# Kernel optimization log

Hardware: AMD Instinct MI355X
Metric: run time of the kernel (lower is better)

Reference implementation:

```python
import jax, jax.numpy as jnp
import numpy as np

H = 2048      # hidden_size
DM = 4096     # intermediate_size
N = 16        # ssm state size
K = 4         # conv kernel
R = 128       # time_step_rank
B_SZ = 1
L = 1024


def setup_inputs() -> dict:
    key = jax.random.key(0)
    ks = jax.random.split(key, 10)
    s = 0.02
    hidden_states = jax.random.normal(ks[0], (B_SZ, L, H), dtype=jnp.float32)
    W_in = jax.random.normal(ks[1], (2 * DM, H), dtype=jnp.float32) * s
    conv_w = jax.random.normal(ks[2], (DM, 1, K), dtype=jnp.float32) * 0.3
    conv_b = jax.random.normal(ks[3], (DM,), dtype=jnp.float32) * 0.1
    W_x = jax.random.normal(ks[4], (R + 2 * N, DM), dtype=jnp.float32) * s
    W_dt = jax.random.normal(ks[5], (DM, R), dtype=jnp.float32) * s
    b_dt = jax.random.normal(ks[6], (DM,), dtype=jnp.float32) * 0.1
    # A_log init: log(arange(1..N)) broadcast over channels (per __init__)
    A_log = jnp.broadcast_to(jnp.log(jnp.arange(1, N + 1, dtype=jnp.float32))[None, :], (DM, N)).copy()
    D_param = jnp.ones((DM,), dtype=jnp.float32)
    W_out = jax.random.normal(ks[7], (H, DM), dtype=jnp.float32) * s
    return {"hidden_states": hidden_states, "W_in": W_in, "conv_w": conv_w,
            "conv_b": conv_b, "W_x": W_x, "W_dt": W_dt, "b_dt": b_dt,
            "A_log": A_log, "D_param": D_param, "W_out": W_out}


def reference(hidden_states, W_in, conv_w, conv_b, W_x, W_dt, b_dt, A_log, D_param, W_out):
    # in_proj then chunk into hidden / gate (torch chunks dim=1 after transpose)
    proj = hidden_states @ W_in.T                     # [B, L, 2D]
    h, gate = proj[..., :DM], proj[..., DM:]          # each [B, L, D]
    # depthwise causal conv1d, padding K-1 then truncate to L (left-pad == same)
    h_cl = jnp.transpose(h, (0, 2, 1))                # [B, D, L]
    hc = jax.lax.conv_general_dilated(
        h_cl, conv_w, window_strides=(1,), padding=[(K - 1, 0)],
        dimension_numbers=("NCH", "OIH", "NCH"), feature_group_count=DM)
    hc = jax.nn.silu(hc + conv_b[None, :, None])      # [B, D, L]
    hc_ld = jnp.transpose(hc, (0, 2, 1))              # [B, L, D]
    # x_proj -> dt, B, C
    ssm_p = hc_ld @ W_x.T                             # [B, L, R+2N]
    ts, Bm, Cm = ssm_p[..., :R], ssm_p[..., R:R + N], ssm_p[..., R + N:]
    dt = jax.nn.softplus(ts @ W_dt.T + b_dt)          # [B, L, D]
    A = -jnp.exp(A_log)                               # [D, N]
    dA = jnp.exp(dt[:, :, :, None] * A[None, None, :, :])            # [B, L, D, N]
    dBu = dt[:, :, :, None] * Bm[:, :, None, :] * hc_ld[:, :, :, None]  # [B, L, D, N]
    # selective scan over time: state = dA*state + dBu; y = <state, C>
    def step(state, inp):
        dA_t, dBu_t, C_t = inp                        # [B,D,N],[B,D,N],[B,N]
        state = dA_t * state + dBu_t
        y = jnp.einsum("bdn,bn->bd", state, C_t)
        return state, y
    init = jnp.zeros((hidden_states.shape[0], DM, N), dtype=hidden_states.dtype)
    _, ys = jax.lax.scan(step, init,
                         (jnp.swapaxes(dA, 0, 1), jnp.swapaxes(dBu, 0, 1), jnp.swapaxes(Cm, 0, 1)))
    y = jnp.transpose(ys, (1, 0, 2))                  # [B, L, D]
    y = y + hc_ld * D_param[None, None, :]            # skip via D
    y = y * jax.nn.silu(gate)                         # gating
    return y @ W_out.T                                # [B, L, H]
```

## Files before the change

kernel.cpp:

```cpp
#include <hip/hip_runtime.h>
#include <math.h>

#define AS1 __attribute__((address_space(1)))
#define AS3 __attribute__((address_space(3)))

typedef __attribute__((ext_vector_type(8))) short short8;
typedef __attribute__((ext_vector_type(4))) float f32x4;

#define WAITV(n) asm volatile("s_waitcnt vmcnt(" #n ")" ::: "memory")
#define LGKM0()  asm volatile("s_waitcnt lgkmcnt(0)" ::: "memory")
#define BARRIER() asm volatile("s_barrier" ::: "memory")
#define SCHEDB() __builtin_amdgcn_sched_barrier(0)

static __device__ __forceinline__ unsigned short f2bf(float f) {
    unsigned u = __float_as_uint(f);
    unsigned r = (u + 0x7fffu + ((u >> 16) & 1u)) >> 16;
    return (unsigned short)r;
}
static __device__ __forceinline__ float bf2f(unsigned short u) {
    return __uint_as_float(((unsigned)u) << 16);
}

__global__ __launch_bounds__(256) void cvt_f32_bf16(const float* __restrict__ src,
                                                    unsigned short* __restrict__ dst,
                                                    int n4) {
    int i = blockIdx.x * 256 + threadIdx.x;
    int stride = gridDim.x * 256;
    for (; i < n4; i += stride) {
        float4 v = ((const float4*)src)[i];
        ushort4 o;
        o.x = f2bf(v.x); o.y = f2bf(v.y); o.z = f2bf(v.z); o.w = f2bf(v.w);
        ((ushort4*)dst)[i] = o;
    }
}

__global__ __launch_bounds__(256) void cvt_ts(const float* __restrict__ ssmp,
                                              unsigned short* __restrict__ ts) {
    int i = blockIdx.x * 256 + threadIdx.x;
    int t = i >> 5, c4 = (i & 31) * 4;
    float4 v = *(const float4*)&ssmp[t * 160 + c4];
    ushort4 o;
    o.x = f2bf(v.x); o.y = f2bf(v.y); o.z = f2bf(v.z); o.w = f2bf(v.w);
    *(ushort4*)&ts[t * 128 + c4] = o;
}

__global__ __launch_bounds__(256) void conv_silu(const float* __restrict__ h,
                                                 const float* __restrict__ cw,
                                                 const float* __restrict__ cb,
                                                 unsigned short* __restrict__ hc_bf) {
    int idx = blockIdx.x * 256 + threadIdx.x;
    int d = idx & 4095, t = idx >> 12;
    float acc = cb[d];
    float4 w = *(const float4*)&cw[d * 4];
    const float* wp = (const float*)&w;
#pragma unroll
    for (int k = 0; k < 4; ++k) {
        int tt = t + k - 3;
        if (tt >= 0) acc += h[tt * 4096 + d] * wp[k];
    }
    float s = acc / (1.f + __expf(-acc));
    hc_bf[idx] = f2bf(s);
}

__global__ __launch_bounds__(256) void reduce4(const float* __restrict__ pA,
                                               const float* __restrict__ pB,
                                               float* __restrict__ out, int n4) {
    int i = blockIdx.x * 256 + threadIdx.x;
    int stride = gridDim.x * 256;
    const size_t MN4 = (size_t)1024 * 2048 / 4;
    for (; i < n4; i += stride) {
        float4 a = ((const float4*)pA)[i];
        float4 b = ((const float4*)pA)[i + MN4];
        float4 c = ((const float4*)pB)[i];
        float4 d = ((const float4*)pB)[i + MN4];
        float4 o;
        o.x = (a.x + b.x) + (c.x + d.x);
        o.y = (a.y + b.y) + (c.y + d.y);
        o.z = (a.z + b.z) + (c.z + d.z);
        o.w = (a.w + b.w) + (c.w + d.w);
        ((float4*)out)[i] = o;
    }
}

enum { P_GATE = 0, P_PART = 1 };

template <int EPI>
__global__ __launch_bounds__(512, 2)
void gemm8p(const short* __restrict__ A, const short* __restrict__ B,
            void* __restrict__ C0v, void* __restrict__ C1v,
            int N, int K, int kchunk) {
    __shared__ short lds[3 * 24576];

    const int tid = threadIdx.x;
    const int wv = tid >> 6, ln = tid & 63;
    const int lr = ln & 15, kg = ln >> 4;
    const int wm = wv >> 2, wn = wv & 3;

    const int nwg = gridDim.x;
    const int bid = blockIdx.x;
    const int swz = (bid & 7) * (nwg >> 3) + (bid >> 3);
    const int by = swz & 7, bx = swz >> 3;
    const int m0 = by * 128;
    const int n0 = bx * 256;
    const int kbeg = blockIdx.z * kchunk;
    const int NT = kchunk >> 6;

    f32x4 acc[4][4];
#pragma unroll
    for (int mi = 0; mi < 4; ++mi)
#pragma unroll
        for (int ni = 0; ni < 4; ++ni) acc[mi][ni] = (f32x4){0.f, 0.f, 0.f, 0.f};

    const short* Abase = A + (size_t)m0 * K + kbeg;
    const short* Bbase = B + (size_t)n0 * K + kbeg;

#define STAGE_A(kt, b)                                                        \
    {                                                                         \
        short* lbase = &lds[(b) * 24576];                                     \
        _Pragma("unroll")                                                     \
        for (int r = 0; r < 2; ++r) {                                         \
            int c = r * 512 + tid;                                            \
            int row = c >> 3, cb8 = (c & 7) << 4;                             \
            int scb = cb8 ^ ((row & 7) << 4);                                 \
            const short* src = Abase + (size_t)row * K + (kt) * 64 + (scb >> 1); \
            short* dst = lbase + (r * 512 + wv * 64) * 8;                     \
            __builtin_amdgcn_global_load_lds((const AS1 void*)src,            \
                                             (AS3 void*)dst, 16, 0, 0);       \
        }                                                                     \
    }
#define STAGE_B(kt, b, r0)                                                    \
    {                                                                         \
        short* lbase = &lds[(b) * 24576];                                     \
        _Pragma("unroll")                                                     \
        for (int r = (r0); r < (r0) + 2; ++r) {                               \
            int c = r * 512 + tid;                                            \
            int row = c >> 3, cb8 = (c & 7) << 4;                             \
            int scb = cb8 ^ ((row & 7) << 4);                                 \
            const short* src = Bbase + (size_t)row * K + (kt) * 64 + (scb >> 1); \
            short* dst = lbase + 8192 + (r * 512 + wv * 64) * 8;              \
            __builtin_amdgcn_global_load_lds((const AS1 void*)src,            \
                                             (AS3 void*)dst, 16, 0, 0);       \
        }                                                                     \
    }
#define RD_A(dst, mi, ks)                                                     \
    { int row = wm * 64 + (mi) * 16 + lr;                                     \
      int col = ((ks) * 32 + kg * 8) ^ ((row & 7) << 3);                      \
      dst = *(const short8*)&la[row * 64 + col]; }
#define RD_B(dst, ni, ks)                                                     \
    { int row = wn * 64 + (ni) * 16 + lr;                                     \
      int col = ((ks) * 32 + kg * 8) ^ ((row & 7) << 3);                      \
      dst = *(const short8*)&lb[row * 64 + col]; }
#define MFMA4(mi, a)                                                          \
    acc[mi][0] = __builtin_amdgcn_mfma_f32_16x16x32_bf16(a, vb0, acc[mi][0], 0, 0, 0); \
    acc[mi][1] = __builtin_amdgcn_mfma_f32_16x16x32_bf16(a, vb1, acc[mi][1], 0, 0, 0); \
    acc[mi][2] = __builtin_amdgcn_mfma_f32_16x16x32_bf16(a, vb2, acc[mi][2], 0, 0, 0); \
    acc[mi][3] = __builtin_amdgcn_mfma_f32_16x16x32_bf16(a, vb3, acc[mi][3], 0, 0, 0);

    STAGE_A(0, 0); STAGE_B(0, 0, 0); STAGE_B(0, 0, 2);
    if (NT > 1) { STAGE_A(1, 1); STAGE_B(1, 1, 0); STAGE_B(1, 1, 2); }

    for (int kt = 0; kt < NT; ++kt) {
        const int b = kt % 3;
        const int bnx = (kt + 2) % 3;
        const bool pf = (kt + 2 < NT);
        if (kt + 1 < NT) { WAITV(6); } else { WAITV(0); }
        BARRIER();
        const short* la = &lds[b * 24576];
        const short* lb = la + 8192;
        short8 vb0, vb1, vb2, vb3, va0, va1;
        RD_B(vb0, 0, 0); RD_B(vb1, 1, 0); RD_B(vb2, 2, 0); RD_B(vb3, 3, 0);
        RD_A(va0, 0, 0); RD_A(va1, 1, 0);
        if (pf) STAGE_A(kt + 2, bnx);
        LGKM0(); SCHEDB();
        __builtin_amdgcn_s_setprio(1);
        MFMA4(0, va0); MFMA4(1, va1);
        __builtin_amdgcn_s_setprio(0); SCHEDB();
        BARRIER();
        RD_A(va0, 2, 0); RD_A(va1, 3, 0);
        if (pf) STAGE_B(kt + 2, bnx, 0);
        LGKM0(); SCHEDB();
        __builtin_amdgcn_s_setprio(1);
        MFMA4(2, va0); MFMA4(3, va1);
        __builtin_amdgcn_s_setprio(0); SCHEDB();
        BARRIER();
        RD_B(vb0, 0, 1); RD_B(vb1, 1, 1); RD_B(vb2, 2, 1); RD_B(vb3, 3, 1);
        RD_A(va0, 0, 1); RD_A(va1, 1, 1);
        if (pf) STAGE_B(kt + 2, bnx, 2);
        LGKM0(); SCHEDB();
        __builtin_amdgcn_s_setprio(1);
        MFMA4(0, va0); MFMA4(1, va1);
        __builtin_amdgcn_s_setprio(0); SCHEDB();
        BARRIER();
        RD_A(va0, 2, 1); RD_A(va1, 3, 1);
        LGKM0(); SCHEDB();
        __builtin_amdgcn_s_setprio(1);
        MFMA4(2, va0); MFMA4(3, va1);
        __builtin_amdgcn_s_setprio(0); SCHEDB();
        BARRIER();
    }
#undef STAGE_A
#undef STAGE_B
#undef RD_A
#undef RD_B
#undef MFMA4

#pragma unroll
    for (int mi = 0; mi < 4; ++mi) {
        int crow0 = m0 + wm * 64 + mi * 16 + kg * 4;
#pragma unroll
        for (int ni = 0; ni < 4; ++ni) {
            int ccol = n0 + wn * 64 + ni * 16 + lr;
#pragma unroll
            for (int i = 0; i < 4; ++i) {
                float v = acc[mi][ni][i];
                size_t crow = (size_t)(crow0 + i);
                if constexpr (EPI == P_GATE) {
                    if (ccol < 4096) ((float*)C0v)[crow * 4096 + ccol] = v;
                    else {
                        float s = v / (1.f + __expf(-v));
                        ((unsigned short*)C1v)[crow * 4096 + (ccol - 4096)] = f2bf(s);
                    }
                } else {
                    float* P = (float*)(blockIdx.z < 2 ? C0v : C1v) +
                               (size_t)(blockIdx.z & 1) * 1024 * 2048;
                    P[crow * N + ccol] = v;
                }
            }
        }
    }
}

enum { EPI_PLAIN = 0, EPI_SPLIT = 1, EPI_ATOMIC = 2, EPI_SOFTPLUS = 3 };

template <int BM, int EPI>
__global__ __launch_bounds__(256)
void gemm_bt(const short* __restrict__ A, const short* __restrict__ B,
             float* __restrict__ C, float* __restrict__ C2,
             const float* __restrict__ bias,
             int M, int N, int K, int ldc, int kcLen) {
    __shared__ short A_lds[BM * 32];
    __shared__ short B_lds[128 * 32];
    const int tid = threadIdx.x;
    const int wv = tid >> 6, ln = tid & 63;
    const int lr = ln & 15, kg = ln >> 4;
    const int m0 = blockIdx.y * BM;
    const int n0 = blockIdx.x * 128;
    const int kbeg = blockIdx.z * kcLen;
    const int kend = kbeg + kcLen;
    const int wm = wv >> 1, wn = wv & 1;
    constexpr int MR = BM / 32;

    f32x4 acc[MR][4];
#pragma unroll
    for (int mi = 0; mi < MR; ++mi)
#pragma unroll
        for (int ni = 0; ni < 4; ++ni) acc[mi][ni] = (f32x4){0.f, 0.f, 0.f, 0.f};

    const int arow = tid >> 2;
    const int kq8 = (tid & 3) * 8;

    for (int k0 = kbeg; k0 < kend; k0 += 32) {
#pragma unroll
        for (int r = 0; r < BM / 64; ++r) {
            const short* srcA = A + (size_t)(m0 + r * 64 + arow) * K + (k0 + kq8);
            short* dstA = &A_lds[(r * 64 + wv * 16) * 32];
            __builtin_amdgcn_global_load_lds((const AS1 void*)srcA, (AS3 void*)dstA, 16, 0, 0);
        }
#pragma unroll
        for (int r = 0; r < 2; ++r) {
            int brow = n0 + r * 64 + arow;
            if (brow > N - 1) brow = N - 1;
            const short* srcB = B + (size_t)brow * K + (k0 + kq8);
            short* dstB = &B_lds[(r * 64 + wv * 16) * 32];
            __builtin_amdgcn_global_load_lds((const AS1 void*)srcB, (AS3 void*)dstB, 16, 0, 0);
        }
        __syncthreads();

        short8 av[MR], bv[4];
#pragma unroll
        for (int mi = 0; mi < MR; ++mi)
            av[mi] = *(const short8*)&A_lds[(wm * (BM / 2) + mi * 16 + lr) * 32 + kg * 8];
#pragma unroll
        for (int ni = 0; ni < 4; ++ni)
            bv[ni] = *(const short8*)&B_lds[(wn * 64 + ni * 16 + lr) * 32 + kg * 8];
#pragma unroll
        for (int mi = 0; mi < MR; ++mi)
#pragma unroll
            for (int ni = 0; ni < 4; ++ni)
                acc[mi][ni] = __builtin_amdgcn_mfma_f32_16x16x32_bf16(av[mi], bv[ni], acc[mi][ni], 0, 0, 0);
        __syncthreads();
    }

#pragma unroll
    for (int mi = 0; mi < MR; ++mi) {
        int crow0 = m0 + wm * (BM / 2) + mi * 16 + kg * 4;
#pragma unroll
        for (int ni = 0; ni < 4; ++ni) {
            int ccol = n0 + wn * 64 + ni * 16 + lr;
#pragma unroll
            for (int i = 0; i < 4; ++i) {
                float v = acc[mi][ni][i];
                size_t crow = (size_t)(crow0 + i);
                if constexpr (EPI == EPI_PLAIN) {
                    C[crow * ldc + ccol] = v;
                } else if constexpr (EPI == EPI_SPLIT) {
                    if (ccol < 4096) C[crow * 4096 + ccol] = v;
                    else C2[crow * 4096 + (ccol - 4096)] = v;
                } else if constexpr (EPI == EPI_ATOMIC) {
                    if (ccol < N) atomicAdd(&C[crow * ldc + ccol], v);
                } else {
                    float x = v + bias[ccol];
                    float sp = fmaxf(x, 0.f) + log1pf(__expf(-fabsf(x)));
                    ((unsigned short*)C)[crow * ldc + ccol] = f2bf(sp);
                }
            }
        }
    }
}

#define CLEN 16
#define NCH 64

__global__ __launch_bounds__(256)
void scan_p1(const unsigned short* __restrict__ dt, const unsigned short* __restrict__ hc,
             const float* __restrict__ ssmp, const float* __restrict__ A_log,
             float* __restrict__ Sbuf, float* __restrict__ dtsum) {
    const int tid = threadIdx.x;
    const int c = blockIdx.x & (NCH - 1);
    const int db = blockIdx.x >> 6;
    const int d = db * 256 + tid;
    const int t0 = c * CLEN;

    float Ac[16];
#pragma unroll
    for (int i = 0; i < 4; ++i) {
        float4 v = *(const float4*)&A_log[d * 16 + i * 4];
        Ac[i*4+0] = -__expf(v.x); Ac[i*4+1] = -__expf(v.y);
        Ac[i*4+2] = -__expf(v.z); Ac[i*4+3] = -__expf(v.w);
    }

    __shared__ float sB[CLEN][16];
    sB[tid >> 4][tid & 15] = ssmp[(t0 + (tid >> 4)) * 160 + 128 + (tid & 15)];
    __syncthreads();

    float st[16];
#pragma unroll
    for (int n = 0; n < 16; ++n) st[n] = 0.f;
    float ds = 0.f;

    for (int tt = 0; tt < CLEN; ++tt) {
        size_t g = (size_t)(t0 + tt) * 4096 + d;
        float dtv = bf2f(dt[g]);
        float hcv = bf2f(hc[g]);
        float du = dtv * hcv;
        ds += dtv;
#pragma unroll
        for (int n = 0; n < 16; ++n) {
            float dA = __expf(dtv * Ac[n]);
            st[n] = fmaf(dA, st[n], du * sB[tt][n]);
        }
    }

    float* o = Sbuf + ((size_t)c * 4096 + d) * 16;
#pragma unroll
    for (int i = 0; i < 4; ++i)
        *(float4*)&o[i * 4] = make_float4(st[i*4], st[i*4+1], st[i*4+2], st[i*4+3]);
    dtsum[c * 4096 + d] = ds;
}

__global__ __launch_bounds__(256)
void scan_p2(const float* __restrict__ A_log, const float* __restrict__ dtsum,
             float* __restrict__ S) {
    const int idx = blockIdx.x * 256 + threadIdx.x;
    const int d = idx >> 4;
    const float Ac = -__expf(A_log[idx]);

    float sl[NCH], Pv[NCH];
#pragma unroll
    for (int c = 0; c < NCH; ++c) sl[c] = S[(size_t)c * 65536 + idx];
#pragma unroll
    for (int c = 0; c < NCH; ++c) Pv[c] = __expf(Ac * dtsum[c * 4096 + d]);

    float s = 0.f;
#pragma unroll
    for (int c = 0; c < NCH; ++c) {
        S[(size_t)c * 65536 + idx] = s;
        s = fmaf(Pv[c], s, sl[c]);
    }
}

__global__ __launch_bounds__(256)
void scan_p3(const unsigned short* __restrict__ dt, const unsigned short* __restrict__ hc,
             const float* __restrict__ ssmp, const float* __restrict__ A_log,
             const float* __restrict__ Dp, const unsigned short* __restrict__ gate,
             const float* __restrict__ Sinit, unsigned short* __restrict__ y_bf) {
    const int tid = threadIdx.x;
    const int c = blockIdx.x & (NCH - 1);
    const int db = blockIdx.x >> 6;
    const int d = db * 256 + tid;
    const int t0 = c * CLEN;

    float Ac[16];
#pragma unroll
    for (int i = 0; i < 4; ++i) {
        float4 v = *(const float4*)&A_log[d * 16 + i * 4];
        Ac[i*4+0] = -__expf(v.x); Ac[i*4+1] = -__expf(v.y);
        Ac[i*4+2] = -__expf(v.z); Ac[i*4+3] = -__expf(v.w);
    }
    const float Dcoef = Dp[d];

    __shared__ float sB[CLEN][16], sC[CLEN][16];
    {
        int tt = tid >> 4, nn = tid & 15;
        sB[tt][nn] = ssmp[(t0 + tt) * 160 + 128 + nn];
        sC[tt][nn] = ssmp[(t0 + tt) * 160 + 144 + nn];
    }
    __syncthreads();

    float st[16];
    {
        const float* si = Sinit + ((size_t)c * 4096 + d) * 16;
#pragma unroll
        for (int i = 0; i < 4; ++i) {
            float4 v = *(const float4*)&si[i * 4];
            st[i*4] = v.x; st[i*4+1] = v.y; st[i*4+2] = v.z; st[i*4+3] = v.w;
        }
    }

    for (int tt = 0; tt < CLEN; ++tt) {
        size_t g = (size_t)(t0 + tt) * 4096 + d;
        float dtv = bf2f(dt[g]);
        float hcv = bf2f(hc[g]);
        float du = dtv * hcv;
        float p[16];
#pragma unroll
        for (int n = 0; n < 16; ++n) {
            float dA = __expf(dtv * Ac[n]);
            st[n] = fmaf(dA, st[n], du * sB[tt][n]);
            p[n] = st[n] * sC[tt][n];
        }
#pragma unroll
        for (int n = 0; n < 8; ++n) p[n] += p[n + 8];
#pragma unroll
        for (int n = 0; n < 4; ++n) p[n] += p[n + 4];
        p[0] += p[2]; p[1] += p[3];
        float csum = p[0] + p[1];
        float gv = bf2f(gate[g]);
        float yv = (csum + hcv * Dcoef) * gv;
        y_bf[g] = f2bf(yv);
    }
}

extern "C" void kernel_launch(void* const* d_in, const int* in_sizes, int n_in,
                              void* d_out, int out_size, void* d_ws, size_t ws_size,
                              hipStream_t stream) {
    (void)in_sizes; (void)n_in; (void)out_size; (void)ws_size;
    const float* hidden = (const float*)d_in[0];
    const float* W_in   = (const float*)d_in[1];
    const float* conv_w = (const float*)d_in[2];
    const float* conv_b = (const float*)d_in[3];
    const float* W_x    = (const float*)d_in[4];
    const float* W_dt   = (const float*)d_in[5];
    const float* b_dt   = (const float*)d_in[6];
    const float* A_log  = (const float*)d_in[7];
    const float* D_p    = (const float*)d_in[8];
    const float* W_out  = (const float*)d_in[9];
    float* out = (float*)d_out;

    char* w = (char*)d_ws;
    unsigned short* hid_bf = (unsigned short*)w;  w += (size_t)1024 * 2048 * 2;
    unsigned short* Wbig   = (unsigned short*)w;  w += (size_t)8192 * 2048 * 2;
    float* h_buf           = (float*)w;           w += (size_t)1024 * 4096 * 4;
    unsigned short* gate_bf= (unsigned short*)w;  w += (size_t)1024 * 4096 * 2;
    unsigned short* hc_bf  = (unsigned short*)w;  w += (size_t)1024 * 4096 * 2;
    unsigned short* dt_bf  = (unsigned short*)w;  w += (size_t)1024 * 4096 * 2;
    float* ssmp            = (float*)w;           w += (size_t)1024 * 160 * 4;
    unsigned short* ts_bf  = (unsigned short*)w;  w += (size_t)1024 * 128 * 2;
    unsigned short* Wx_bf  = (unsigned short*)w;  w += (size_t)160 * 4096 * 2;
    unsigned short* Wdt_bf = (unsigned short*)w;  w += (size_t)4096 * 128 * 2;
    unsigned short* y_bf   = (unsigned short*)w;  w += (size_t)1024 * 4096 * 2;
    float* Sbuf            = (float*)w;           w += (size_t)NCH * 4096 * 16 * 4;
    float* dtsum           = (float*)w;           w += (size_t)NCH * 4096 * 4;

    hipMemsetAsync(ssmp, 0, (size_t)1024 * 160 * 4, stream);

    cvt_f32_bf16<<<2048, 256, 0, stream>>>(hidden, hid_bf, 1024 * 2048 / 4);
    cvt_f32_bf16<<<4096, 256, 0, stream>>>(W_in, Wbig, 8192 * 2048 / 4);
    cvt_f32_bf16<<<640, 256, 0, stream>>>(W_x, Wx_bf, 160 * 4096 / 4);
    cvt_f32_bf16<<<512, 256, 0, stream>>>(W_dt, Wdt_bf, 4096 * 128 / 4);

    gemm8p<P_GATE><<<dim3(256, 1, 1), 512, 0, stream>>>(
        (const short*)hid_bf, (const short*)Wbig, h_buf, gate_bf, 8192, 2048, 2048);

    conv_silu<<<16384, 256, 0, stream>>>(h_buf, conv_w, conv_b, hc_bf);

    cvt_f32_bf16<<<2048, 256, 0, stream>>>(W_out, Wbig, 2048 * 4096 / 4);

    gemm_bt<128, EPI_ATOMIC><<<dim3(2, 8, 16), 256, 0, stream>>>(
        (const short*)hc_bf, (const short*)Wx_bf, ssmp, nullptr, nullptr,
        1024, 160, 4096, 160, 256);

    cvt_ts<<<128, 256, 0, stream>>>(ssmp, ts_bf);

    gemm_bt<128, EPI_SOFTPLUS><<<dim3(32, 8, 1), 256, 0, stream>>>(
        (const short*)ts_bf, (const short*)Wdt_bf, (float*)dt_bf, nullptr, b_dt,
        1024, 4096, 128, 4096, 128);

    scan_p1<<<NCH * 16, 256, 0, stream>>>(dt_bf, hc_bf, ssmp, A_log, Sbuf, dtsum);
    scan_p2<<<256, 256, 0, stream>>>(A_log, dtsum, Sbuf);
    scan_p3<<<NCH * 16, 256, 0, stream>>>(dt_bf, hc_bf, ssmp, A_log, D_p, gate_bf, Sbuf, y_bf);

    gemm8p<P_PART><<<dim3(64, 1, 4), 512, 0, stream>>>(
        (const short*)y_bf, (const short*)Wbig, Sbuf, h_buf, 2048, 4096, 1024);
    reduce4<<<2048, 256, 0, stream>>>(Sbuf, h_buf, out, 1024 * 2048 / 4);
}
```

Baseline: 216.2 us.

## Simplify GEMM main loop to one barrier per k-tile with bulk staging

Replaces the four-phase interleaved GEMM inner loop with a simpler schedule. Each k-tile now has a single barrier, then one merged STAGE macro issues all A and B global-to-LDS loads for tile kt+2. After that, all eight A/B fragments are read and sixteen MFMAs are issued per half-k step. The aim is to cut the barrier, lgkmcnt-wait and sched_barrier overhead and let the compiler overlap LDS reads with MFMAs. In exchange it loses the hand-tuned interleaving of global prefetch with compute and holds more fragment registers live. The second prefetch stage is now unconditional, so a k-tile count of 1 would read past the chunk.

```diff
diff --git a/kernel.cpp b/kernel.cpp
--- a/kernel.cpp
+++ b/kernel.cpp
@@ -8,9 +8,7 @@
 typedef __attribute__((ext_vector_type(4))) float f32x4;
 
 #define WAITV(n) asm volatile("s_waitcnt vmcnt(" #n ")" ::: "memory")
-#define LGKM0()  asm volatile("s_waitcnt lgkmcnt(0)" ::: "memory")
 #define BARRIER() asm volatile("s_barrier" ::: "memory")
-#define SCHEDB() __builtin_amdgcn_sched_barrier(0)
 
 static __device__ __forceinline__ unsigned short f2bf(float f) {
     unsigned u = __float_as_uint(f);
@@ -114,7 +112,7 @@
     const short* Abase = A + (size_t)m0 * K + kbeg;
     const short* Bbase = B + (size_t)n0 * K + kbeg;
 
-#define STAGE_A(kt, b)                                                        \
+#define STAGE(kt, b)                                                          \
     {                                                                         \
         short* lbase = &lds[(b) * 24576];                                     \
         _Pragma("unroll")                                                     \
@@ -127,12 +125,8 @@
             __builtin_amdgcn_global_load_lds((const AS1 void*)src,            \
                                              (AS3 void*)dst, 16, 0, 0);       \
         }                                                                     \
-    }
-#define STAGE_B(kt, b, r0)                                                    \
-    {                                                                         \
-        short* lbase = &lds[(b) * 24576];                                     \
         _Pragma("unroll")                                                     \
-        for (int r = (r0); r < (r0) + 2; ++r) {                               \
+        for (int r = 0; r < 4; ++r) {                                         \
             int c = r * 512 + tid;                                            \
             int row = c >> 3, cb8 = (c & 7) << 4;                             \
             int scb = cb8 ^ ((row & 7) << 4);                                 \
@@ -156,50 +150,30 @@
     acc[mi][2] = __builtin_amdgcn_mfma_f32_16x16x32_bf16(a, vb2, acc[mi][2], 0, 0, 0); \
     acc[mi][3] = __builtin_amdgcn_mfma_f32_16x16x32_bf16(a, vb3, acc[mi][3], 0, 0, 0);
 
-    STAGE_A(0, 0); STAGE_B(0, 0, 0); STAGE_B(0, 0, 2);
-    if (NT > 1) { STAGE_A(1, 1); STAGE_B(1, 1, 0); STAGE_B(1, 1, 2); }
+    STAGE(0, 0);
+    STAGE(1, 1);
 
     for (int kt = 0; kt < NT; ++kt) {
         const int b = kt % 3;
-        const int bnx = (kt + 2) % 3;
-        const bool pf = (kt + 2 < NT);
         if (kt + 1 < NT) { WAITV(6); } else { WAITV(0); }
         BARRIER();
+        if (kt + 2 < NT) STAGE(kt + 2, (kt + 2) % 3);
+
         const short* la = &lds[b * 24576];
         const short* lb = la + 8192;
-        short8 vb0, vb1, vb2, vb3, va0, va1;
+        short8 va0, va1, va2, va3, vb0, vb1, vb2, vb3;
         RD_B(vb0, 0, 0); RD_B(vb1, 1, 0); RD_B(vb2, 2, 0); RD_B(vb3, 3, 0);
-        RD_A(va0, 0, 0); RD_A(va1, 1, 0);
-        if (pf) STAGE_A(kt + 2, bnx);
-        LGKM0(); SCHEDB();
+        RD_A(va0, 0, 0); RD_A(va1, 1, 0); RD_A(va2, 2, 0); RD_A(va3, 3, 0);
         __builtin_amdgcn_s_setprio(1);
-        MFMA4(0, va0); MFMA4(1, va1);
-        __builtin_amdgcn_s_setprio(0); SCHEDB();
-        BARRIER();
-        RD_A(va0, 2, 0); RD_A(va1, 3, 0);
-        if (pf) STAGE_B(kt + 2, bnx, 0);
-        LGKM0(); SCHEDB();
+        MFMA4(0, va0); MFMA4(1, va1); MFMA4(2, va2); MFMA4(3, va3);
+        __builtin_amdgcn_s_setprio(0);
+        RD_B(vb0, 0, 1); RD_B(vb1, 1, 1); RD_B(vb2, 2, 1); RD_B(vb3, 3, 1);
+        RD_A(va0, 0, 1); RD_A(va1, 1, 1); RD_A(va2, 2, 1); RD_A(va3, 3, 1);
         __builtin_amdgcn_s_setprio(1);
-        MFMA4(2, va0); MFMA4(3, va1);
-        __builtin_amdgcn_s_setprio(0); SCHEDB();
-        BARRIER();
-        RD_B(vb0, 0, 1); RD_B(vb1, 1, 1); RD_B(vb2, 2, 1); RD_B(vb3, 3, 1);
-        RD_A(va0, 0, 1); RD_A(va1, 1, 1);
-        if (pf) STAGE_B(kt + 2, bnx, 2);
-        LGKM0(); SCHEDB();
-        __builtin_amdgcn_s_setprio(1);
-        MFMA4(0, va0); MFMA4(1, va1);
-        __builtin_amdgcn_s_setprio(0); SCHEDB();
-        BARRIER();
-        RD_A(va0, 2, 1); RD_A(va1, 3, 1);
-        LGKM0(); SCHEDB();
-        __builtin_amdgcn_s_setprio(1);
-        MFMA4(2, va0); MFMA4(3, va1);
-        __builtin_amdgcn_s_setprio(0); SCHEDB();
-        BARRIER();
-    }
-#undef STAGE_A
-#undef STAGE_B
+        MFMA4(0, va0); MFMA4(1, va1); MFMA4(2, va2); MFMA4(3, va3);
+        __builtin_amdgcn_s_setprio(0);
+    }
+#undef STAGE
 #undef RD_A
 #undef RD_B
 #undef MFMA4
```

New measurement: 216.1 us. Within noise of the previous version (-0.0%).
